# Kernel tuning notes

Hardware: AMD Instinct MI355X
Metric: run time of the kernel (lower is better)

Reference implementation:

```python
import jax, jax.numpy as jnp
import numpy as np

N = 100000      # nodes
E = 1600000     # edges
IN = 128        # in_channels
HEADS = 4
HID = 32        # hidden_channels (per-head dim)
HD = HEADS * HID  # 128, concat output dim
OUT = 2         # out_channels


def setup_inputs() -> dict:
    key = jax.random.key(0)
    ks = jax.random.split(key, 18)

    def lin(kw, kb, fan_in, fan_out):
        lim = 1.0 / np.sqrt(fan_in)
        W = jax.random.uniform(kw, (fan_in, fan_out), jnp.float32, -lim, lim)
        b = jax.random.uniform(kb, (fan_out,), jnp.float32, -lim, lim)
        return W, b

    x = jax.random.normal(ks[0], (N, IN), jnp.float32)
    edge_index = jax.random.randint(ks[1], (2, E), 0, N, jnp.int32)

    Wq, bq = lin(ks[2], ks[3], IN, HD)   # lin_query
    Wk, bk = lin(ks[4], ks[5], IN, HD)   # lin_key
    Wv, bv = lin(ks[6], ks[7], IN, HD)   # lin_value
    Ws, bs = lin(ks[8], ks[9], IN, HD)   # lin_skip (root weight)
    W1, b1 = lin(ks[10], ks[11], HD, 6 * HEADS)  # readout Linear(128, 24)
    W2, b2 = lin(ks[12], ks[13], 6 * HEADS, 8)   # readout Linear(24, 8)
    W3, b3 = lin(ks[14], ks[15], 8, OUT)         # readout Linear(8, 2)

    return {"x": x, "edge_index": edge_index,
            "Wq": Wq, "bq": bq, "Wk": Wk, "bk": bk, "Wv": Wv, "bv": bv,
            "Ws": Ws, "bs": bs, "W1": W1, "b1": b1, "W2": W2, "b2": b2,
            "W3": W3, "b3": b3}


def _tanhshrink(z):
    return z - jnp.tanh(z)


def reference(x, edge_index, Wq, bq, Wk, bk, Wv, bv, Ws, bs,
              W1, b1, W2, b2, W3, b3):
    n = x.shape[0]
    src, dst = edge_index[0], edge_index[1]  # messages flow src -> dst

    # TransformerConv: per-node Q/K/V projections, reshaped to heads
    q = (x @ Wq + bq).reshape(n, HEADS, HID)
    k = (x @ Wk + bk).reshape(n, HEADS, HID)
    v = (x @ Wv + bv).reshape(n, HEADS, HID)

    # per-edge gather + attention logits [E, H]
    scale = 1.0 / np.float32(np.sqrt(HID))
    scores = jnp.einsum('ehd,ehd->eh', q[dst], k[src]) * scale

    # segment softmax over incoming edges of each dst node (numerically stable)
    m = jax.ops.segment_max(scores, dst, num_segments=n)
    m = jnp.where(jnp.isfinite(m), m, 0.0)  # guard isolated nodes
    e = jnp.exp(scores - m[dst])
    denom = jax.ops.segment_sum(e, dst, num_segments=n)
    alpha = e / denom[dst]  # [E, H]

    # weighted scatter-aggregate of values, concat heads, add root skip
    agg = jax.ops.segment_sum(alpha[:, :, None] * v[src], dst,
                              num_segments=n).reshape(n, HD)
    h = jnp.tanh(agg + x @ Ws + bs)  # bn() in source is an identity reshape

    # readout MLP (Dropout p=0.01 omitted: eval mode)
    h1 = _tanhshrink(h @ W1 + b1)
    h2 = _tanhshrink(h1 @ W2 + b2)
    return h2 @ W3 + b3
```

## Files before the change

kernel.cpp:

```cpp
#include <hip/hip_runtime.h>
#include <hip/hip_bf16.h>
#include <hip/hip_fp16.h>
#include <math.h>

#define NN 100000
#define EE 1600000
#define HD_ 128
#define PART 8
#define RNG 12500
#define PBLK 128
#define PSTRIDE (PBLK * 256)
#define CAP 64

typedef float f32x4 __attribute__((ext_vector_type(4)));
typedef _Float16 f16x8 __attribute__((ext_vector_type(8)));
typedef _Float16 f16x2 __attribute__((ext_vector_type(2)));
typedef float accf4 __attribute__((ext_vector_type(4)));

__device__ __forceinline__ float fast_tanh(float z) {
    float az = fabsf(z);
    float e = __expf(-2.f * az);
    float t = (1.f - e) / (1.f + e);
    return copysignf(t, z);
}

struct alignas(16) h8 { __half2 h[4]; };
struct alignas(8)  h4 { __half2 a, b; };

__global__ __launch_bounds__(256) void wt_kernel(
    const float* __restrict__ Wq, const float* __restrict__ Wk,
    const float* __restrict__ Wv, const float* __restrict__ Ws,
    __half* __restrict__ Wt)
{
    const int t = blockIdx.x * 256 + threadIdx.x;
    const int lane = t & 63;
    const int kt = (t >> 6) & 3;
    const int ct = (t >> 8) & 7;
    const int mat = t >> 11;
    const float* Wm = (mat == 0) ? Wq : (mat == 1) ? Wk : (mat == 2) ? Wv : Ws;
    const int col = ct * 16 + (lane & 15);
    const int k0 = kt * 32 + (lane >> 4) * 8;
    h8 hh;
#pragma unroll
    for (int j = 0; j < 4; ++j) {
        hh.h[j] = __floats2half2_rn(Wm[(size_t)(k0 + 2 * j) * 128 + col],
                                    Wm[(size_t)(k0 + 2 * j + 1) * 128 + col]);
    }
    *reinterpret_cast<h8*>(Wt + (size_t)t * 8) = hh;
}

__global__ __launch_bounds__(256) void proj_mfma(
    const float* __restrict__ x, const __half* __restrict__ Wt,
    const float* __restrict__ bq, const float* __restrict__ bk,
    const float* __restrict__ bv, const float* __restrict__ bs,
    __half* __restrict__ Qh, __half* __restrict__ Sh, __half* __restrict__ KV)
{
    __shared__ __half xs[16][136];
    __shared__ __half ys[16][520];
    const int tid = threadIdx.x;
    const int n0 = blockIdx.x * 16;

    {
        const int row = tid & 15;
        const int k0 = (tid >> 4) * 8;
        const f32x4* xp = reinterpret_cast<const f32x4*>(
            x + (size_t)(n0 + row) * 128 + k0);
        f32x4 a = __builtin_nontemporal_load(xp);
        f32x4 b = __builtin_nontemporal_load(xp + 1);
        h8 hh;
        hh.h[0] = __floats2half2_rn(a.x, a.y);
        hh.h[1] = __floats2half2_rn(a.z, a.w);
        hh.h[2] = __floats2half2_rn(b.x, b.y);
        hh.h[3] = __floats2half2_rn(b.z, b.w);
        *reinterpret_cast<h8*>(&xs[row][k0]) = hh;
    }
    __syncthreads();

    const int w = tid >> 6;
    const int lane = tid & 63;
    const float* bm = (w == 0) ? bq : (w == 1) ? bk : (w == 2) ? bv : bs;
    const float sc = (w == 0) ? 0.17677669529663687f : 1.f;

    f16x8 bx[4];
#pragma unroll
    for (int kt = 0; kt < 4; ++kt)
        bx[kt] = *reinterpret_cast<const f16x8*>(
            &xs[lane & 15][kt * 32 + (lane >> 4) * 8]);

    const __half* wbase = Wt + (size_t)w * 16384;

#pragma unroll
    for (int ct = 0; ct < 8; ++ct) {
        accf4 acc = {0.f, 0.f, 0.f, 0.f};
#pragma unroll
        for (int kt = 0; kt < 4; ++kt) {
            f16x8 af = *reinterpret_cast<const f16x8*>(
                wbase + (size_t)((ct * 4 + kt) * 64 + lane) * 8);
            acc = __builtin_amdgcn_mfma_f32_16x16x32_f16(af, bx[kt], acc, 0, 0, 0);
        }
        const float4 bb = *reinterpret_cast<const float4*>(
            bm + ct * 16 + ((lane >> 4) << 2));
        h4 o;
        o.a = __floats2half2_rn((acc[0] + bb.x) * sc, (acc[1] + bb.y) * sc);
        o.b = __floats2half2_rn((acc[2] + bb.z) * sc, (acc[3] + bb.w) * sc);
        *reinterpret_cast<h4*>(
            &ys[lane & 15][w * 128 + ct * 16 + ((lane >> 4) << 2)]) = o;
    }
    __syncthreads();

    {
        const int node = tid >> 4;
        const int c8 = (tid & 15) * 8;
        h8 q = *reinterpret_cast<h8*>(&ys[node][c8]);
        h8 k = *reinterpret_cast<h8*>(&ys[node][128 + c8]);
        h8 v = *reinterpret_cast<h8*>(&ys[node][256 + c8]);
        h8 s = *reinterpret_cast<h8*>(&ys[node][384 + c8]);
        *reinterpret_cast<h8*>(Qh + (size_t)(n0 + node) * 128 + c8) = q;
        *reinterpret_cast<h8*>(KV + (size_t)(n0 + node) * 256 + c8) = k;
        *reinterpret_cast<h8*>(KV + (size_t)(n0 + node) * 256 + 128 + c8) = v;
        *reinterpret_cast<h8*>(Sh + (size_t)(n0 + node) * 128 + c8) = s;
    }
}

__global__ __launch_bounds__(256) void bucket_scatter(
    const int* __restrict__ ei, int* __restrict__ cnt, int* __restrict__ ssrc)
{
    const int g = blockIdx.x & (PART - 1);
    const int bg = blockIdx.x >> 3;
    const int lo = g * RNG;
    const int hi = lo + RNG;
    for (int e = bg * 256 + threadIdx.x; e < EE; e += PSTRIDE) {
        const int d = ei[EE + e];
        if (d >= lo && d < hi) {
            int pos = atomicAdd(&cnt[d], 1);
            if (pos < CAP) ssrc[(d << 6) | pos] = ei[e];
        }
    }
}

__global__ __launch_bounds__(256) void attn_kernel(
    const __half* __restrict__ Qh, const __half* __restrict__ KV,
    const __half* __restrict__ Sh,
    const int* __restrict__ cnt, const int* __restrict__ ssrc,
    __half* __restrict__ hbuf)
{
    const int wid = threadIdx.x >> 6;
    const int lane = threadIdx.x & 63;
    const int node = blockIdx.x * 4 + wid;
    const int eg = lane >> 4;
    const int li = lane & 15;

    h8 qq = *reinterpret_cast<const h8*>(Qh + (size_t)node * 128 + li * 8);
    f16x2 qp[4];
#pragma unroll
    for (int j = 0; j < 4; ++j)
        qp[j] = *reinterpret_cast<const f16x2*>(&qq.h[j]);

    float a[8];
#pragma unroll
    for (int j = 0; j < 8; ++j) a[j] = 0.f;
    float l = 0.f;

    const int st = node << 6;
    int dg = cnt[node];
    if (dg > CAP) dg = CAP;

    for (int it = 0; it < dg; it += 16) {
        const __half* rows[4];
        bool val[4];
#pragma unroll
        for (int b = 0; b < 4; ++b) {
            const int e = it + b * 4 + eg;
            val[b] = e < dg;
            const int src = ssrc[st + (val[b] ? e : 0)];
            rows[b] = KV + (size_t)src * 256 + li * 8;
        }

        h8 kk[4], vv[4];
#pragma unroll
        for (int b = 0; b < 4; ++b) {
            kk[b] = *reinterpret_cast<const h8*>(rows[b]);
            vv[b] = *reinterpret_cast<const h8*>(rows[b] + 128);
        }

        float p[4];
#pragma unroll
        for (int b = 0; b < 4; ++b) {
            float s = 0.f;
#if __has_builtin(__builtin_amdgcn_fdot2)
#pragma unroll
            for (int j = 0; j < 4; ++j)
                s = __builtin_amdgcn_fdot2(
                        qp[j], *reinterpret_cast<const f16x2*>(&kk[b].h[j]),
                        s, false);
#else
#pragma unroll
            for (int j = 0; j < 4; ++j) {
                const float2 kf = __half22float2(kk[b].h[j]);
                const float2 qf = __half22float2(qq.h[j]);
                s = fmaf(qf.x, kf.x, s);
                s = fmaf(qf.y, kf.y, s);
            }
#endif
            p[b] = s;
        }

#pragma unroll
        for (int b = 0; b < 4; ++b) {
            p[b] += __shfl_xor(p[b], 1);
            p[b] += __shfl_xor(p[b], 2);
        }

        float w[4];
#pragma unroll
        for (int b = 0; b < 4; ++b) {
            w[b] = val[b] ? __expf(p[b]) : 0.f;
            l += w[b];
        }

#pragma unroll
        for (int b = 0; b < 4; ++b) {
#pragma unroll
            for (int j = 0; j < 4; ++j) {
                const float2 vf = __half22float2(vv[b].h[j]);
                a[2 * j]     = fmaf(w[b], vf.x, a[2 * j]);
                a[2 * j + 1] = fmaf(w[b], vf.y, a[2 * j + 1]);
            }
        }
    }

#pragma unroll
    for (int j = 0; j < 8; ++j) {
        a[j] += __shfl_xor(a[j], 16);
        a[j] += __shfl_xor(a[j], 32);
    }
    l += __shfl_xor(l, 16);
    l += __shfl_xor(l, 32);

    const float inv = (l > 0.f) ? 1.f / l : 0.f;

    if (eg == 0) {
        const h8 ss = *reinterpret_cast<const h8*>(Sh + (size_t)node * 128 + li * 8);
        h8 ho;
#pragma unroll
        for (int j = 0; j < 4; ++j) {
            const float2 sf = __half22float2(ss.h[j]);
            const float h0 = fast_tanh(a[2 * j] * inv + sf.x);
            const float h1 = fast_tanh(a[2 * j + 1] * inv + sf.y);
            ho.h[j] = __floats2half2_rn(h0, h1);
        }
        *reinterpret_cast<h8*>(hbuf + (size_t)node * 128 + li * 8) = ho;
    }
}

__global__ __launch_bounds__(256) void mlp_kernel(
    const __half* __restrict__ hbuf,
    const float* __restrict__ W1, const float* __restrict__ b1,
    const float* __restrict__ W2, const float* __restrict__ b2,
    const float* __restrict__ W3, const float* __restrict__ b3,
    float* __restrict__ out)
{
    __shared__ float W1s[128][24];
    __shared__ float W2s[24][8];
    __shared__ float W3s[8][2];
    __shared__ float b1s[24], b2s[8], b3s[2];

    const int tid = threadIdx.x;

    {
        const float4* src = reinterpret_cast<const float4*>(W1 + tid * 12);
        float4* dst = reinterpret_cast<float4*>(&W1s[0][0] + tid * 12);
        dst[0] = src[0];
        dst[1] = src[1];
        dst[2] = src[2];
        if (tid < 48)
            reinterpret_cast<float4*>(&W2s[0][0])[tid] =
                reinterpret_cast<const float4*>(W2)[tid];
        if (tid < 4)
            reinterpret_cast<float4*>(&W3s[0][0])[tid] =
                reinterpret_cast<const float4*>(W3)[tid];
        if (tid < 24) b1s[tid] = b1[tid];
        if (tid < 8)  b2s[tid] = b2[tid];
        if (tid < 2)  b3s[tid] = b3[tid];
    }
    __syncthreads();

    const int node = blockIdx.x * 256 + tid;
    if (node >= NN) return;

    float t24[24];
#pragma unroll
    for (int j = 0; j < 24; ++j) t24[j] = b1s[j];

    const h8* hrow = reinterpret_cast<const h8*>(hbuf + (size_t)node * 128);
#pragma unroll
    for (int c = 0; c < 16; ++c) {
        const h8 hh = hrow[c];
        float hf[8];
#pragma unroll
        for (int j = 0; j < 4; ++j) {
            const float2 f = __half22float2(hh.h[j]);
            hf[2 * j] = f.x;
            hf[2 * j + 1] = f.y;
        }
#pragma unroll
        for (int i = 0; i < 8; ++i) {
            const int kk = c * 8 + i;
#pragma unroll
            for (int j4 = 0; j4 < 6; ++j4) {
                const float4 w4 = *reinterpret_cast<const float4*>(&W1s[kk][j4 * 4]);
                t24[j4 * 4 + 0] = fmaf(hf[i], w4.x, t24[j4 * 4 + 0]);
                t24[j4 * 4 + 1] = fmaf(hf[i], w4.y, t24[j4 * 4 + 1]);
                t24[j4 * 4 + 2] = fmaf(hf[i], w4.z, t24[j4 * 4 + 2]);
                t24[j4 * 4 + 3] = fmaf(hf[i], w4.w, t24[j4 * 4 + 3]);
            }
        }
    }

    float u8[8];
#pragma unroll
    for (int j = 0; j < 8; ++j) u8[j] = b2s[j];
#pragma unroll
    for (int kk = 0; kk < 24; ++kk) {
        const float hv = t24[kk] - fast_tanh(t24[kk]);
#pragma unroll
        for (int j = 0; j < 8; ++j) u8[j] = fmaf(hv, W2s[kk][j], u8[j]);
    }

    float o0 = b3s[0], o1 = b3s[1];
#pragma unroll
    for (int kk = 0; kk < 8; ++kk) {
        const float hv = u8[kk] - fast_tanh(u8[kk]);
        o0 = fmaf(hv, W3s[kk][0], o0);
        o1 = fmaf(hv, W3s[kk][1], o1);
    }
    *reinterpret_cast<float2*>(out + (size_t)node * 2) = make_float2(o0, o1);
}

extern "C" void kernel_launch(void* const* d_in, const int* in_sizes, int n_in,
                              void* d_out, int out_size, void* d_ws, size_t ws_size,
                              hipStream_t stream)
{
    const float* x  = (const float*)d_in[0];
    const int*   ei = (const int*)d_in[1];
    const float* Wq = (const float*)d_in[2];
    const float* bq = (const float*)d_in[3];
    const float* Wk = (const float*)d_in[4];
    const float* bk = (const float*)d_in[5];
    const float* Wv = (const float*)d_in[6];
    const float* bv = (const float*)d_in[7];
    const float* Ws = (const float*)d_in[8];
    const float* bs = (const float*)d_in[9];
    const float* W1 = (const float*)d_in[10];
    const float* b1 = (const float*)d_in[11];
    const float* W2 = (const float*)d_in[12];
    const float* b2 = (const float*)d_in[13];
    const float* W3 = (const float*)d_in[14];
    const float* b3 = (const float*)d_in[15];
    float* out = (float*)d_out;

    __half* ws = (__half*)d_ws;
    __half* Qh = ws;
    __half* Sh = Qh + (size_t)NN * HD_;
    __half* KV = Sh + (size_t)NN * HD_;
    __half* hbuf = KV + (size_t)NN * 256;
    __half* Wt = hbuf + (size_t)NN * HD_;
    int* cnt  = (int*)(Wt + 65536);
    int* ssrc = cnt + NN;

    (void)hipMemsetAsync(cnt, 0, NN * sizeof(int), stream);

    wt_kernel<<<32, 256, 0, stream>>>(Wq, Wk, Wv, Ws, Wt);
    proj_mfma<<<NN / 16, 256, 0, stream>>>(x, Wt, bq, bk, bv, bs, Qh, Sh, KV);
    bucket_scatter<<<PART * PBLK, 256, 0, stream>>>(ei, cnt, ssrc);
    attn_kernel<<<NN / 4, 256, 0, stream>>>(Qh, KV, Sh, cnt, ssrc, hbuf);
    mlp_kernel<<<(NN + 255) / 256, 256, 0, stream>>>(hbuf, W1, b1, W2, b2,
                                                     W3, b3, out);
}
```

Before: 281.2 us.

## Make projection kernel persistent with register-resident weights and prefetched x tiles

```diff
diff --git a/kernel.cpp b/kernel.cpp
--- a/kernel.cpp
+++ b/kernel.cpp
@@ -9,8 +9,11 @@
 #define PART 8
 #define RNG 12500
 #define PBLK 128
+#define SCATB (PART * PBLK)
 #define PSTRIDE (PBLK * 256)
 #define CAP 64
+#define PROJ_GRID 512
+#define NTILES (NN / 16)
 
 typedef float f32x4 __attribute__((ext_vector_type(4)));
 typedef _Float16 f16x8 __attribute__((ext_vector_type(8)));
@@ -58,67 +61,89 @@
     __shared__ __half xs[16][136];
     __shared__ __half ys[16][520];
     const int tid = threadIdx.x;
-    const int n0 = blockIdx.x * 16;
-
-    {
-        const int row = tid & 15;
-        const int k0 = (tid >> 4) * 8;
-        const f32x4* xp = reinterpret_cast<const f32x4*>(
-            x + (size_t)(n0 + row) * 128 + k0);
-        f32x4 a = __builtin_nontemporal_load(xp);
-        f32x4 b = __builtin_nontemporal_load(xp + 1);
-        h8 hh;
-        hh.h[0] = __floats2half2_rn(a.x, a.y);
-        hh.h[1] = __floats2half2_rn(a.z, a.w);
-        hh.h[2] = __floats2half2_rn(b.x, b.y);
-        hh.h[3] = __floats2half2_rn(b.z, b.w);
-        *reinterpret_cast<h8*>(&xs[row][k0]) = hh;
-    }
-    __syncthreads();
-
     const int w = tid >> 6;
     const int lane = tid & 63;
+
+    f16x8 wf[32];
+    {
+        const __half* wbase = Wt + (size_t)w * 16384;
+#pragma unroll
+        for (int i = 0; i < 32; ++i)
+            wf[i] = *reinterpret_cast<const f16x8*>(
+                wbase + (size_t)(i * 64 + lane) * 8);
+    }
+
     const float* bm = (w == 0) ? bq : (w == 1) ? bk : (w == 2) ? bv : bs;
     const float sc = (w == 0) ? 0.17677669529663687f : 1.f;
 
-    f16x8 bx[4];
-#pragma unroll
-    for (int kt = 0; kt < 4; ++kt)
-        bx[kt] = *reinterpret_cast<const f16x8*>(
-            &xs[lane & 15][kt * 32 + (lane >> 4) * 8]);
-
-    const __half* wbase = Wt + (size_t)w * 16384;
-
-#pragma unroll
-    for (int ct = 0; ct < 8; ++ct) {
-        accf4 acc = {0.f, 0.f, 0.f, 0.f};
-#pragma unroll
-        for (int kt = 0; kt < 4; ++kt) {
-            f16x8 af = *reinterpret_cast<const f16x8*>(
-                wbase + (size_t)((ct * 4 + kt) * 64 + lane) * 8);
-            acc = __builtin_amdgcn_mfma_f32_16x16x32_f16(af, bx[kt], acc, 0, 0, 0);
-        }
-        const float4 bb = *reinterpret_cast<const float4*>(
-            bm + ct * 16 + ((lane >> 4) << 2));
-        h4 o;
-        o.a = __floats2half2_rn((acc[0] + bb.x) * sc, (acc[1] + bb.y) * sc);
-        o.b = __floats2half2_rn((acc[2] + bb.z) * sc, (acc[3] + bb.w) * sc);
-        *reinterpret_cast<h4*>(
-            &ys[lane & 15][w * 128 + ct * 16 + ((lane >> 4) << 2)]) = o;
-    }
-    __syncthreads();
-
-    {
-        const int node = tid >> 4;
-        const int c8 = (tid & 15) * 8;
-        h8 q = *reinterpret_cast<h8*>(&ys[node][c8]);
-        h8 k = *reinterpret_cast<h8*>(&ys[node][128 + c8]);
-        h8 v = *reinterpret_cast<h8*>(&ys[node][256 + c8]);
-        h8 s = *reinterpret_cast<h8*>(&ys[node][384 + c8]);
-        *reinterpret_cast<h8*>(Qh + (size_t)(n0 + node) * 128 + c8) = q;
-        *reinterpret_cast<h8*>(KV + (size_t)(n0 + node) * 256 + c8) = k;
-        *reinterpret_cast<h8*>(KV + (size_t)(n0 + node) * 256 + 128 + c8) = v;
-        *reinterpret_cast<h8*>(Sh + (size_t)(n0 + node) * 128 + c8) = s;
+    const int srow = tid & 15;
+    const int sk0 = (tid >> 4) * 8;
+
+    int t = blockIdx.x;
+    f32x4 ra, rb;
+    if (t < NTILES) {
+        const f32x4* xp = reinterpret_cast<const f32x4*>(
+            x + (size_t)(t * 16 + srow) * 128 + sk0);
+        ra = __builtin_nontemporal_load(xp);
+        rb = __builtin_nontemporal_load(xp + 1);
+    }
+
+    for (; t < NTILES; t += PROJ_GRID) {
+        const int n0 = t * 16;
+
+        {
+            h8 hh;
+            hh.h[0] = __floats2half2_rn(ra.x, ra.y);
+            hh.h[1] = __floats2half2_rn(ra.z, ra.w);
+            hh.h[2] = __floats2half2_rn(rb.x, rb.y);
+            hh.h[3] = __floats2half2_rn(rb.z, rb.w);
+            *reinterpret_cast<h8*>(&xs[srow][sk0]) = hh;
+        }
+        __syncthreads();
+
+        if (t + PROJ_GRID < NTILES) {
+            const f32x4* xp = reinterpret_cast<const f32x4*>(
+                x + (size_t)((t + PROJ_GRID) * 16 + srow) * 128 + sk0);
+            ra = __builtin_nontemporal_load(xp);
+            rb = __builtin_nontemporal_load(xp + 1);
+        }
+
+        f16x8 bx[4];
+#pragma unroll
+        for (int kt = 0; kt < 4; ++kt)
+            bx[kt] = *reinterpret_cast<const f16x8*>(
+                &xs[lane & 15][kt * 32 + (lane >> 4) * 8]);
+
+#pragma unroll
+        for (int ct = 0; ct < 8; ++ct) {
+            accf4 acc = {0.f, 0.f, 0.f, 0.f};
+#pragma unroll
+            for (int kt = 0; kt < 4; ++kt)
+                acc = __builtin_amdgcn_mfma_f32_16x16x32_f16(
+                    wf[ct * 4 + kt], bx[kt], acc, 0, 0, 0);
+            const float4 bb = *reinterpret_cast<const float4*>(
+                bm + ct * 16 + ((lane >> 4) << 2));
+            h4 o;
+            o.a = __floats2half2_rn((acc[0] + bb.x) * sc, (acc[1] + bb.y) * sc);
+            o.b = __floats2half2_rn((acc[2] + bb.z) * sc, (acc[3] + bb.w) * sc);
+            *reinterpret_cast<h4*>(
+                &ys[lane & 15][w * 128 + ct * 16 + ((lane >> 4) << 2)]) = o;
+        }
+        __syncthreads();
+
+        {
+            const int node = tid >> 4;
+            const int c8 = (tid & 15) * 8;
+            h8 q = *reinterpret_cast<h8*>(&ys[node][c8]);
+            h8 k = *reinterpret_cast<h8*>(&ys[node][128 + c8]);
+            h8 v = *reinterpret_cast<h8*>(&ys[node][256 + c8]);
+            h8 s = *reinterpret_cast<h8*>(&ys[node][384 + c8]);
+            *reinterpret_cast<h8*>(Qh + (size_t)(n0 + node) * 128 + c8) = q;
+            *reinterpret_cast<h8*>(KV + (size_t)(n0 + node) * 256 + c8) = k;
+            *reinterpret_cast<h8*>(KV + (size_t)(n0 + node) * 256 + 128 + c8) = v;
+            *reinterpret_cast<h8*>(Sh + (size_t)(n0 + node) * 128 + c8) = s;
+        }
+        __syncthreads();
     }
 }
 
@@ -371,8 +396,8 @@
     (void)hipMemsetAsync(cnt, 0, NN * sizeof(int), stream);
 
     wt_kernel<<<32, 256, 0, stream>>>(Wq, Wk, Wv, Ws, Wt);
-    proj_mfma<<<NN / 16, 256, 0, stream>>>(x, Wt, bq, bk, bv, bs, Qh, Sh, KV);
-    bucket_scatter<<<PART * PBLK, 256, 0, stream>>>(ei, cnt, ssrc);
+    bucket_scatter<<<SCATB, 256, 0, stream>>>(ei, cnt, ssrc);
+    proj_mfma<<<PROJ_GRID, 256, 0, stream>>>(x, Wt, bq, bk, bv, bs, Qh, Sh, KV);
     attn_kernel<<<NN / 4, 256, 0, stream>>>(Qh, KV, Sh, cnt, ssrc, hbuf);
     mlp_kernel<<<(NN + 255) / 256, 256, 0, stream>>>(hbuf, W1, b1, W2, b2,
                                                      W3, b3, out);
```

After: 254.5 us. 1.11x faster.
